# Performance work log

Hardware: AMD Instinct MI355X
Metric: run time of the kernel (lower is better)

Reference implementation:

```python
import jax, jax.numpy as jnp
import numpy as np

T, B, I, H = 512, 64, 1024, 1024


def setup_inputs() -> dict:
    key = jax.random.key(0)
    ks = jax.random.split(key, 7)
    s = 1.0 / np.sqrt(H)
    return {
        "x": jax.random.normal(ks[0], (T, B, I), jnp.float32),
        "h0": jax.random.normal(ks[1], (B, H), jnp.float32),
        "c0": jax.random.normal(ks[2], (B, H), jnp.float32),
        "W_ih": jax.random.normal(ks[3], (4 * H, I), jnp.float32) * s,
        "W_hh": jax.random.normal(ks[4], (4 * H, H), jnp.float32) * s,
        "b_ih": jax.random.normal(ks[5], (4 * H,), jnp.float32) * s,
        "b_hh": jax.random.normal(ks[6], (4 * H,), jnp.float32) * s,
    }


def reference(x, h0, c0, W_ih, W_hh, b_ih, b_hh):
    # Precompute input-to-gate projections for all timesteps at once (same math,
    # just hoisted out of the recurrence): [T, B, 4H]
    gx = jnp.einsum("tbi,gi->tbg", x, W_ih) + b_ih + b_hh

    def step(carry, gx_t):
        h, c = carry
        gates = gx_t + h @ W_hh.T  # [B, 4H]
        i, f, g, o = jnp.split(gates, 4, axis=-1)  # torch LSTMCell gate order
        i = jax.nn.sigmoid(i)
        f = jax.nn.sigmoid(f)
        g = jnp.tanh(g)
        o = jax.nn.sigmoid(o)
        c_new = f * c + i * g
        h_new = o * jnp.tanh(c_new)
        return (h_new, c_new), h_new

    (h_fin, c_fin), outputs = jax.lax.scan(step, (h0, c0), gx)
    return outputs, h_fin, c_fin
```

## Files before the change

### kernel.cpp

```cpp
#include <hip/hip_runtime.h>
#include <hip/hip_bf16.h>


#define BH 65536

typedef __attribute__((ext_vector_type(8))) short bf16x8;
typedef __attribute__((ext_vector_type(4))) float f32x4;

__device__ inline ushort f2bf(float x) {
    __hip_bfloat16 b = __float2bfloat16(x);
    return *(ushort*)&b;
}
__device__ inline float bf2f(ushort u) {
    __hip_bfloat16 b = *(__hip_bfloat16*)&u;
    return __bfloat162float(b);
}

__device__ inline bf16x8 ldh16(const ushort* p) {
    union { unsigned long long q[2]; bf16x8 v; } u;
    u.q[0] = __hip_atomic_load((const unsigned long long*)p,
                               __ATOMIC_RELAXED, __HIP_MEMORY_SCOPE_AGENT);
    u.q[1] = __hip_atomic_load((const unsigned long long*)(p + 4),
                               __ATOMIC_RELAXED, __HIP_MEMORY_SCOPE_AGENT);
    return u.v;
}

__global__ void split_bf16(const float* __restrict__ src,
                           ushort* __restrict__ hi, ushort* __restrict__ lo,
                           long n)
{
    long i0 = ((long)blockIdx.x * blockDim.x + threadIdx.x) * 4;
    long stride = (long)gridDim.x * blockDim.x * 4;
    for (long e = i0; e < n; e += stride) {
        float4 v = *(const float4*)(src + e);
        ushort4 hv, lv;
        hv.x = f2bf(v.x); lv.x = f2bf(v.x - bf2f(hv.x));
        hv.y = f2bf(v.y); lv.y = f2bf(v.y - bf2f(hv.y));
        hv.z = f2bf(v.z); lv.z = f2bf(v.z - bf2f(hv.z));
        hv.w = f2bf(v.w); lv.w = f2bf(v.w - bf2f(hv.w));
        *(ushort4*)(hi + e) = hv;
        *(ushort4*)(lo + e) = lv;
    }
}

__global__ __launch_bounds__(256)
void gx_mfma(const ushort* __restrict__ xhi, const ushort* __restrict__ xlo,
             const ushort* __restrict__ whi, const ushort* __restrict__ wlo,
             const float* __restrict__ bih, const float* __restrict__ bhh,
             float* __restrict__ gxp)
{
    __shared__ short lds[4][4096];
    const int tid  = threadIdx.x;
    const int lane = tid & 63;
    const int w    = tid >> 6;
    const int wm   = w >> 1, wn = w & 1;
    const int mt0  = blockIdx.y * 128;
    const int nt0  = blockIdx.x * 128;

    const int lr_ = w * 16 + (lane >> 2);
    const int lc_ = (lane & 3) * 8;

    f32x4 acc[4][4] = {};

    for (int kt = 0; kt < 1024; kt += 32) {
        uint4 rah[2], ral[2], rbh[2], rbl[2];
        #pragma unroll
        for (int s = 0; s < 2; ++s) {
            size_t ao = (size_t)(mt0 + s * 64 + lr_) * 1024 + kt + lc_;
            size_t bo = (size_t)(nt0 + s * 64 + lr_) * 1024 + kt + lc_;
            rah[s] = *(const uint4*)(xhi + ao);
            ral[s] = *(const uint4*)(xlo + ao);
            rbh[s] = *(const uint4*)(whi + bo);
            rbl[s] = *(const uint4*)(wlo + bo);
        }
        __syncthreads();
        #pragma unroll
        for (int s = 0; s < 2; ++s) {
            int row = s * 64 + lr_;
            int us  = (lane & 3) ^ ((row >> 1) & 3);
            int off = row * 32 + us * 8;
            *(uint4*)&lds[0][off] = rah[s];
            *(uint4*)&lds[1][off] = ral[s];
            *(uint4*)&lds[2][off] = rbh[s];
            *(uint4*)&lds[3][off] = rbl[s];
        }
        __syncthreads();
        bf16x8 ah[4], al[4], bh[4], bl[4];
        #pragma unroll
        for (int f = 0; f < 4; ++f) {
            int arow = wm * 64 + f * 16 + (lane & 15);
            int brow = wn * 64 + f * 16 + (lane & 15);
            int aus  = (lane >> 4) ^ ((arow >> 1) & 3);
            int bus  = (lane >> 4) ^ ((brow >> 1) & 3);
            int ar = arow * 32 + aus * 8;
            int br = brow * 32 + bus * 8;
            ah[f] = *(bf16x8*)&lds[0][ar];
            al[f] = *(bf16x8*)&lds[1][ar];
            bh[f] = *(bf16x8*)&lds[2][br];
            bl[f] = *(bf16x8*)&lds[3][br];
        }
        #pragma unroll
        for (int i = 0; i < 4; ++i)
            #pragma unroll
            for (int j = 0; j < 4; ++j) {
                acc[i][j] = __builtin_amdgcn_mfma_f32_16x16x32_bf16(ah[i], bh[j], acc[i][j], 0, 0, 0);
                acc[i][j] = __builtin_amdgcn_mfma_f32_16x16x32_bf16(ah[i], bl[j], acc[i][j], 0, 0, 0);
                acc[i][j] = __builtin_amdgcn_mfma_f32_16x16x32_bf16(al[i], bh[j], acc[i][j], 0, 0, 0);
            }
    }
    #pragma unroll
    for (int j = 0; j < 4; ++j) {
        int r = nt0 + wn * 64 + j * 16 + (lane & 15);
        float bias = bih[r] + bhh[r];
        int g = r >> 10, u = r & 1023;
        #pragma unroll
        for (int i = 0; i < 4; ++i) {
            #pragma unroll
            for (int e = 0; e < 4; ++e) {
                int m = mt0 + wm * 64 + i * 16 + (lane >> 4) * 4 + e;
                int trel = m >> 6, b = m & 63;
                gxp[(((size_t)trel * 256 + (u >> 2)) * 64 + b) * 16 + g * 4 + (u & 3)]
                    = acc[i][j][e] + bias;
            }
        }
    }
}

#define BM 128
#define BN 128
#define BKg 16

__global__ __launch_bounds__(256, 2)
void gx_gemm(const float* __restrict__ x, const float* __restrict__ Wih,
             const float* __restrict__ bih, const float* __restrict__ bhh,
             float* __restrict__ gxp, int t0)
{
    __shared__ float As[BKg][BM + 4];
    __shared__ float Bs[BKg][BN + 4];
    const int tid  = threadIdx.x;
    const int nblk = blockIdx.x;
    const int mblk = blockIdx.y;
    const int lrow = tid >> 2;
    const int lkq  = (tid & 3) * 4;
    const int ty   = tid >> 4;
    const int tx   = tid & 15;

    const float* xb = x   + ((size_t)t0 * 64 + (size_t)mblk * BM) * 1024;
    const float* wb = Wih + (size_t)nblk * BN * 1024;

    float acc[8][8] = {};
    for (int kt = 0; kt < 1024; kt += BKg) {
        const int k0 = kt + lkq;
        float4 a0 = *(const float4*)(xb + (size_t)lrow        * 1024 + k0);
        float4 a1 = *(const float4*)(xb + (size_t)(lrow + 64) * 1024 + k0);
        float4 b0 = *(const float4*)(wb + (size_t)lrow        * 1024 + k0);
        float4 b1 = *(const float4*)(wb + (size_t)(lrow + 64) * 1024 + k0);
        __syncthreads();
        As[lkq + 0][lrow] = a0.x; As[lkq + 1][lrow] = a0.y;
        As[lkq + 2][lrow] = a0.z; As[lkq + 3][lrow] = a0.w;
        As[lkq + 0][lrow + 64] = a1.x; As[lkq + 1][lrow + 64] = a1.y;
        As[lkq + 2][lrow + 64] = a1.z; As[lkq + 3][lrow + 64] = a1.w;
        Bs[lkq + 0][lrow] = b0.x; Bs[lkq + 1][lrow] = b0.y;
        Bs[lkq + 2][lrow] = b0.z; Bs[lkq + 3][lrow] = b0.w;
        Bs[lkq + 0][lrow + 64] = b1.x; Bs[lkq + 1][lrow + 64] = b1.y;
        Bs[lkq + 2][lrow + 64] = b1.z; Bs[lkq + 3][lrow + 64] = b1.w;
        __syncthreads();
        #pragma unroll
        for (int kk = 0; kk < BKg; ++kk) {
            float4 af0 = *(float4*)&As[kk][ty * 8];
            float4 af1 = *(float4*)&As[kk][ty * 8 + 4];
            float4 bf0 = *(float4*)&Bs[kk][tx * 8];
            float4 bf1 = *(float4*)&Bs[kk][tx * 8 + 4];
            float a[8] = {af0.x, af0.y, af0.z, af0.w, af1.x, af1.y, af1.z, af1.w};
            float b[8] = {bf0.x, bf0.y, bf0.z, bf0.w, bf1.x, bf1.y, bf1.z, bf1.w};
            #pragma unroll
            for (int i = 0; i < 8; ++i)
                #pragma unroll
                for (int j = 0; j < 8; ++j)
                    acc[i][j] += a[i] * b[j];
        }
    }
    float bias[8];
    #pragma unroll
    for (int j = 0; j < 8; ++j) {
        int r = nblk * BN + tx * 8 + j;
        bias[j] = bih[r] + bhh[r];
    }
    #pragma unroll
    for (int i = 0; i < 8; ++i) {
        int ml   = mblk * BM + ty * 8 + i;
        int trel = ml >> 6, b = ml & 63;
        #pragma unroll
        for (int jj = 0; jj < 2; ++jj) {
            int r = nblk * BN + tx * 8 + jj * 4;
            int g = r >> 10, u = r & 1023;
            float4 v = make_float4(acc[i][jj*4+0] + bias[jj*4+0],
                                   acc[i][jj*4+1] + bias[jj*4+1],
                                   acc[i][jj*4+2] + bias[jj*4+2],
                                   acc[i][jj*4+3] + bias[jj*4+3]);
            *(float4*)(gxp + ((((size_t)trel * 256 + (u >> 2)) * 64 + b) << 4) + g * 4) = v;
        }
    }
}

__device__ inline void flagbar(uint token, uint* flags, uint* gen)
{
    __syncthreads();
    const int tid = threadIdx.x;
    if (blockIdx.x == 0) {
        if (tid == 0)
            __hip_atomic_store(&flags[0], token, __ATOMIC_RELAXED, __HIP_MEMORY_SCOPE_AGENT);
        while (__hip_atomic_load(&flags[tid * 16], __ATOMIC_RELAXED, __HIP_MEMORY_SCOPE_AGENT) < token)
            __builtin_amdgcn_s_sleep(2);
        __syncthreads();
        if (tid < 32)
            __hip_atomic_store(&gen[tid * 16], token, __ATOMIC_RELAXED, __HIP_MEMORY_SCOPE_AGENT);
    } else {
        if (tid == 0) {
            __hip_atomic_store(&flags[blockIdx.x * 16], token, __ATOMIC_RELAXED, __HIP_MEMORY_SCOPE_AGENT);
            uint* myg = &gen[(blockIdx.x & 31) * 16];
            while (__hip_atomic_load(myg, __ATOMIC_RELAXED, __HIP_MEMORY_SCOPE_AGENT) < token)
                __builtin_amdgcn_s_sleep(2);
        }
    }
    __syncthreads();
}

__global__ __launch_bounds__(256, 1)
void lstm_persist(const ushort* __restrict__ whh_hi, const ushort* __restrict__ whh_lo,
                  const float* __restrict__ gxp, ushort* __restrict__ hpl,
                  const float* __restrict__ c0, float* __restrict__ cbuf,
                  float* __restrict__ out, int t0, int chunk, uint* bar)
{
    __shared__ float  part[4][64][20];
    __shared__ ushort hstg[64][8];
    const int tid  = threadIdx.x;
    const int lane = tid & 63;
    const int w    = tid >> 6;
    const int cu   = blockIdx.x;
    uint* flags = bar;
    uint* gen   = bar + 4096;

    const int rl    = lane & 15;
    const size_t wrow = (size_t)((rl >> 2) * 1024 + cu * 4 + (rl & 3)) * 1024;
    const int klane = (lane >> 4) * 8;
    const int kbase = w * 256;
    const int bq    = lane & 15;

    bf16x8 a_hi[8], a_lo[8];
    #pragma unroll
    for (int ks = 0; ks < 8; ++ks) {
        int k0 = kbase + ks * 32 + klane;
        a_hi[ks] = *(const bf16x8*)(whh_hi + wrow + k0);
        a_lo[ks] = *(const bf16x8*)(whh_lo + wrow + k0);
    }

    const int eb = tid >> 2, eu = tid & 3;
    const int hcol = cu * 4 + eu;
    float c_reg = (t0 == 0) ? c0[eb * 1024 + hcol] : cbuf[eb * 1024 + hcol];

    for (int t = t0; t < t0 + chunk; ++t) {
        const ushort* hin_hi = hpl + (size_t)(((t + 1) & 1) * 2 + 0) * BH;
        const ushort* hin_lo = hpl + (size_t)(((t + 1) & 1) * 2 + 1) * BH;

        const float* gx = gxp + (((size_t)(t - t0) * 256 + cu) * 64 + eb) * 16;
        float gxv0 = gx[0 + eu], gxv1 = gx[4 + eu];
        float gxv2 = gx[8 + eu], gxv3 = gx[12 + eu];

        f32x4 acc[4] = {};
        #pragma unroll
        for (int ks = 0; ks < 8; ++ks) {
            int k0 = kbase + ks * 32 + klane;
            #pragma unroll
            for (int nt = 0; nt < 4; ++nt) {
                size_t ho = (size_t)(nt * 16 + bq) * 1024 + k0;
                bf16x8 b_hi = ldh16(hin_hi + ho);
                bf16x8 b_lo = ldh16(hin_lo + ho);
                acc[nt] = __builtin_amdgcn_mfma_f32_16x16x32_bf16(a_hi[ks], b_hi, acc[nt], 0, 0, 0);
                acc[nt] = __builtin_amdgcn_mfma_f32_16x16x32_bf16(a_hi[ks], b_lo, acc[nt], 0, 0, 0);
                acc[nt] = __builtin_amdgcn_mfma_f32_16x16x32_bf16(a_lo[ks], b_hi, acc[nt], 0, 0, 0);
            }
        }
        const int r0 = (lane >> 4) * 4;
        #pragma unroll
        for (int nt = 0; nt < 4; ++nt)
            *(f32x4*)&part[w][nt * 16 + bq][r0] = acc[nt];
        __syncthreads();

        float pre0 = part[0][eb][0  + eu] + part[1][eb][0  + eu] + part[2][eb][0  + eu] + part[3][eb][0  + eu] + gxv0;
        float pre1 = part[0][eb][4  + eu] + part[1][eb][4  + eu] + part[2][eb][4  + eu] + part[3][eb][4  + eu] + gxv1;
        float pre2 = part[0][eb][8  + eu] + part[1][eb][8  + eu] + part[2][eb][8  + eu] + part[3][eb][8  + eu] + gxv2;
        float pre3 = part[0][eb][12 + eu] + part[1][eb][12 + eu] + part[2][eb][12 + eu] + part[3][eb][12 + eu] + gxv3;
        float gi = __fdividef(1.0f, 1.0f + __expf(-pre0));
        float gf = __fdividef(1.0f, 1.0f + __expf(-pre1));
        float gg = 1.0f - __fdividef(2.0f, __expf(2.0f * pre2) + 1.0f);
        float go = __fdividef(1.0f, 1.0f + __expf(-pre3));
        c_reg = gf * c_reg + gi * gg;
        float hn = go * (1.0f - __fdividef(2.0f, __expf(2.0f * c_reg) + 1.0f));

        out[((size_t)t * 64 + eb) * 1024 + hcol] = hn;
        ushort hh = f2bf(hn);
        hstg[eb][eu]     = hh;
        hstg[eb][4 + eu] = f2bf(hn - bf2f(hh));
        if (t == 511) {
            out[(size_t)512 * BH + eb * 1024 + hcol]      = hn;
            out[(size_t)512 * BH + BH + eb * 1024 + hcol] = c_reg;
        }
        __syncthreads();
        if (tid < 128) {
            int eb2 = tid >> 1, jj = tid & 1;
            const uint* row = (const uint*)&hstg[eb2][0];
            ushort* hobase = hpl + (size_t)((t & 1) * 2) * BH + eb2 * 1024 + cu * 4;
            __hip_atomic_store((uint*)hobase + jj,      row[jj],
                               __ATOMIC_RELAXED, __HIP_MEMORY_SCOPE_AGENT);
            __hip_atomic_store((uint*)(hobase + BH) + jj, row[2 + jj],
                               __ATOMIC_RELAXED, __HIP_MEMORY_SCOPE_AGENT);
        }
        flagbar((uint)(t + 1), flags, gen);
    }
    if (t0 + chunk < 512)
        cbuf[eb * 1024 + hcol] = c_reg;
}

__global__ __launch_bounds__(256)
void lstm_step_mfma(const ushort* __restrict__ whh_hi, const ushort* __restrict__ whh_lo,
                    const float* __restrict__ gxp,
                    const ushort* __restrict__ hin_hi, const ushort* __restrict__ hin_lo,
                    const float* __restrict__ cprev, float* __restrict__ cbuf,
                    ushort* __restrict__ hout_hi, ushort* __restrict__ hout_lo,
                    float* __restrict__ out, int t, int trel)
{
    __shared__ float part[4][64][20];
    const int tid  = threadIdx.x;
    const int lane = tid & 63;
    const int w    = tid >> 6;
    const int cu   = blockIdx.x;

    const int rl    = lane & 15;
    const size_t wrow = (size_t)((rl >> 2) * 1024 + cu * 4 + (rl & 3)) * 1024;
    const int klane = (lane >> 4) * 8;
    const int kbase = w * 256;
    const int bq    = lane & 15;

    f32x4 acc[4] = {};
    #pragma unroll
    for (int ks = 0; ks < 8; ++ks) {
        int k0 = kbase + ks * 32 + klane;
        bf16x8 a_hi = *(const bf16x8*)(whh_hi + wrow + k0);
        bf16x8 a_lo = *(const bf16x8*)(whh_lo + wrow + k0);
        #pragma unroll
        for (int nt = 0; nt < 4; ++nt) {
            size_t ho = (size_t)(nt * 16 + bq) * 1024 + k0;
            bf16x8 b_hi = *(const bf16x8*)(hin_hi + ho);
            bf16x8 b_lo = *(const bf16x8*)(hin_lo + ho);
            acc[nt] = __builtin_amdgcn_mfma_f32_16x16x32_bf16(a_hi, b_hi, acc[nt], 0, 0, 0);
            acc[nt] = __builtin_amdgcn_mfma_f32_16x16x32_bf16(a_hi, b_lo, acc[nt], 0, 0, 0);
            acc[nt] = __builtin_amdgcn_mfma_f32_16x16x32_bf16(a_lo, b_hi, acc[nt], 0, 0, 0);
        }
    }
    const int r0 = (lane >> 4) * 4;
    #pragma unroll
    for (int nt = 0; nt < 4; ++nt)
        *(f32x4*)&part[w][nt * 16 + bq][r0] = acc[nt];
    __syncthreads();

    const int eb = tid >> 2, eu = tid & 3;
    const float* gx = gxp + (((size_t)trel * 256 + cu) * 64 + eb) * 16;
    float pre[4];
    #pragma unroll
    for (int g = 0; g < 4; ++g) {
        int r = g * 4 + eu;
        pre[g] = part[0][eb][r] + part[1][eb][r] + part[2][eb][r] + part[3][eb][r]
               + gx[g * 4 + eu];
    }
    float gi = __fdividef(1.0f, 1.0f + __expf(-pre[0]));
    float gf = __fdividef(1.0f, 1.0f + __expf(-pre[1]));
    float gg = 1.0f - __fdividef(2.0f, __expf(2.0f * pre[2]) + 1.0f);
    float go = __fdividef(1.0f, 1.0f + __expf(-pre[3]));
    float c_reg = cprev[eb * 1024 + cu * 4 + eu];
    c_reg = gf * c_reg + gi * gg;
    float hn = go * (1.0f - __fdividef(2.0f, __expf(2.0f * c_reg) + 1.0f));

    int hcol = cu * 4 + eu;
    cbuf[eb * 1024 + hcol] = c_reg;
    out[((size_t)t * 64 + eb) * 1024 + hcol] = hn;
    ushort hh = f2bf(hn);
    hout_hi[eb * 1024 + hcol] = hh;
    hout_lo[eb * 1024 + hcol] = f2bf(hn - bf2f(hh));
    if (t == 511) {
        out[(size_t)512 * BH + eb * 1024 + hcol]      = hn;
        out[(size_t)512 * BH + BH + eb * 1024 + hcol] = c_reg;
    }
}

extern "C" void kernel_launch(void* const* d_in, const int* in_sizes, int n_in,
                              void* d_out, int out_size, void* d_ws, size_t ws_size,
                              hipStream_t stream)
{
    const float* x   = (const float*)d_in[0];
    const float* h0  = (const float*)d_in[1];
    const float* c0  = (const float*)d_in[2];
    const float* Wih = (const float*)d_in[3];
    const float* Whh = (const float*)d_in[4];
    const float* bih = (const float*)d_in[5];
    const float* bhh = (const float*)d_in[6];
    float* out = (float*)d_out;

    char* ws = (char*)d_ws;
    float* cbuf = (float*)ws;

    const size_t FIXED0 = 262144 + 4 * 8388608L + 524288;
    const size_t FIXED  = FIXED0 + 32768;
    const long   PER    = 2 * 131072L + 1048576L;
    long Tc = ((long)ws_size - (long)FIXED) / PER;

    if (Tc >= 2) {
        if (Tc > 512) Tc = 512;
        Tc &= ~1L;
        ushort* wih_hi = (ushort*)(ws + 262144);
        ushort* wih_lo = wih_hi + 4194304;
        ushort* whh_hi = wih_lo + 4194304;
        ushort* whh_lo = whh_hi + 4194304;
        ushort* hpl    = whh_lo + 4194304;
        uint*   bar    = (uint*)(ws + FIXED0);
        char*   var    = ws + FIXED;
        ushort* xhi    = (ushort*)var;
        ushort* xlo    = (ushort*)(var + Tc * 131072);
        float*  gxp    = (float*)(var + Tc * 262144);

        hipMemsetAsync(bar, 0, 32768, stream);
        split_bf16<<<dim3(2048), dim3(256), 0, stream>>>(Wih, wih_hi, wih_lo, 4194304L);
        split_bf16<<<dim3(2048), dim3(256), 0, stream>>>(Whh, whh_hi, whh_lo, 4194304L);
        split_bf16<<<dim3(64),   dim3(256), 0, stream>>>(h0, hpl + 2 * BH, hpl + 3 * BH, (long)BH);

        bool coop_ok = true;
        for (int t0 = 0; t0 < 512; t0 += (int)Tc) {
            int chunk = (512 - t0 < (int)Tc) ? (512 - t0) : (int)Tc;
            split_bf16<<<dim3(4096), dim3(256), 0, stream>>>(
                x + (size_t)t0 * BH, xhi, xlo, (long)chunk * BH);
            gx_mfma<<<dim3(32, chunk / 2), dim3(256), 0, stream>>>(
                xhi, xlo, wih_hi, wih_lo, bih, bhh, gxp);
            if (coop_ok) {
                void* args[] = {(void*)&whh_hi, (void*)&whh_lo, (void*)&gxp,
                                (void*)&hpl, (void*)&c0, (void*)&cbuf,
                                (void*)&out, (void*)&t0, (void*)&chunk,
                                (void*)&bar};
                hipError_t e = hipLaunchCooperativeKernel(
                    (void*)lstm_persist, dim3(256), dim3(256), args, 0, stream);
                if (e != hipSuccess) { (void)hipGetLastError(); coop_ok = false; }
            }
            if (!coop_ok) {
                for (int trel = 0; trel < chunk; ++trel) {
                    int t = t0 + trel;
                    int rb = (t + 1) & 1, wb = t & 1;
                    const float* cp = (t == 0) ? c0 : cbuf;
                    lstm_step_mfma<<<dim3(256), dim3(256), 0, stream>>>(
                        whh_hi, whh_lo, gxp,
                        hpl + rb * 2 * BH, hpl + rb * 2 * BH + BH,
                        cp, cbuf,
                        hpl + wb * 2 * BH, hpl + wb * 2 * BH + BH,
                        out, t, trel);
                }
            }
        }
    } else {
        ushort* whh_hi = (ushort*)(ws + 262144);
        ushort* whh_lo = whh_hi + 4194304;
        ushort* hpl    = whh_lo + 4194304;
        const size_t FIXED2 = 262144 + 2 * 8388608L + 524288;
        float* gxp = (float*)(ws + FIXED2);
        long Tc2 = ((long)ws_size - (long)FIXED2) / 1048576L;
        if (Tc2 > 512) Tc2 = 512;
        Tc2 &= ~1L;
        if (Tc2 < 2) Tc2 = 2;

        split_bf16<<<dim3(2048), dim3(256), 0, stream>>>(Whh, whh_hi, whh_lo, 4194304L);
        split_bf16<<<dim3(64),   dim3(256), 0, stream>>>(h0, hpl + 2 * BH, hpl + 3 * BH, (long)BH);

        for (int t0 = 0; t0 < 512; t0 += (int)Tc2) {
            int chunk = (512 - t0 < (int)Tc2) ? (512 - t0) : (int)Tc2;
            gx_gemm<<<dim3(32, chunk * 64 / BM), dim3(256), 0, stream>>>(
                x, Wih, bih, bhh, gxp, t0);
            for (int trel = 0; trel < chunk; ++trel) {
                int t = t0 + trel;
                int rb = (t + 1) & 1, wb = t & 1;
                const float* cp = (t == 0) ? c0 : cbuf;
                lstm_step_mfma<<<dim3(256), dim3(256), 0, stream>>>(
                    whh_hi, whh_lo, gxp,
                    hpl + rb * 2 * BH, hpl + rb * 2 * BH + BH,
                    cp, cbuf,
                    hpl + wb * 2 * BH, hpl + wb * 2 * BH + BH,
                    out, t, trel);
            }
        }
    }
}
```

Before: 11.59 ms.

## Restructure persistent LSTM kernel to 64 large blocks with LDS-staged hidden state

The persistent recurrence kernel now runs 64 blocks of 1024 threads instead of 256 blocks of 256. Each block owns 16 hidden units across all four gates. Each step, the block cooperatively loads the full bf16 hi/lo hidden state into swizzled shared memory in four quarter-K chunks, prefetching the next chunk while MFMAs run. Weights are streamed from global memory every step rather than held in registers. The grid barrier now involves 64 blocks, which cuts barrier and synchronisation cost and redundant hidden-state reads, at the price of re-reading W_hh each step and more __syncthreads per step.

```diff
diff --git a/kernel.cpp b/kernel.cpp
--- a/kernel.cpp
+++ b/kernel.cpp
@@ -6,6 +6,7 @@
 
 typedef __attribute__((ext_vector_type(8))) short bf16x8;
 typedef __attribute__((ext_vector_type(4))) float f32x4;
+typedef unsigned long long ull;
 
 __device__ inline ushort f2bf(float x) {
     __hip_bfloat16 b = __float2bfloat16(x);
@@ -14,15 +15,6 @@
 __device__ inline float bf2f(ushort u) {
     __hip_bfloat16 b = *(__hip_bfloat16*)&u;
     return __bfloat162float(b);
-}
-
-__device__ inline bf16x8 ldh16(const ushort* p) {
-    union { unsigned long long q[2]; bf16x8 v; } u;
-    u.q[0] = __hip_atomic_load((const unsigned long long*)p,
-                               __ATOMIC_RELAXED, __HIP_MEMORY_SCOPE_AGENT);
-    u.q[1] = __hip_atomic_load((const unsigned long long*)(p + 4),
-                               __ATOMIC_RELAXED, __HIP_MEMORY_SCOPE_AGENT);
-    return u.v;
 }
 
 __global__ void split_bf16(const float* __restrict__ src,
@@ -203,15 +195,17 @@
     }
 }
 
-__device__ inline void flagbar(uint token, uint* flags, uint* gen)
+__device__ inline void flagbar64(uint token, uint* flags, uint* gen)
 {
     __syncthreads();
     const int tid = threadIdx.x;
     if (blockIdx.x == 0) {
         if (tid == 0)
             __hip_atomic_store(&flags[0], token, __ATOMIC_RELAXED, __HIP_MEMORY_SCOPE_AGENT);
-        while (__hip_atomic_load(&flags[tid * 16], __ATOMIC_RELAXED, __HIP_MEMORY_SCOPE_AGENT) < token)
-            __builtin_amdgcn_s_sleep(2);
+        if (tid < 64) {
+            while (__hip_atomic_load(&flags[tid * 16], __ATOMIC_RELAXED, __HIP_MEMORY_SCOPE_AGENT) < token)
+                __builtin_amdgcn_s_sleep(2);
+        }
         __syncthreads();
         if (tid < 32)
             __hip_atomic_store(&gen[tid * 16], token, __ATOMIC_RELAXED, __HIP_MEMORY_SCOPE_AGENT);
@@ -226,100 +220,138 @@
     __syncthreads();
 }
 
-__global__ __launch_bounds__(256, 1)
+__global__ __launch_bounds__(1024, 4)
 void lstm_persist(const ushort* __restrict__ whh_hi, const ushort* __restrict__ whh_lo,
                   const float* __restrict__ gxp, ushort* __restrict__ hpl,
                   const float* __restrict__ c0, float* __restrict__ cbuf,
                   float* __restrict__ out, int t0, int chunk, uint* bar)
 {
-    __shared__ float  part[4][64][20];
-    __shared__ ushort hstg[64][8];
+    __shared__ uint4  hstage[2][2048];
+    __shared__ float  pre[64][65];
+    __shared__ ushort hstg2[64][32];
+
     const int tid  = threadIdx.x;
     const int lane = tid & 63;
-    const int w    = tid >> 6;
+    const int wid  = tid >> 6;
+    const int g    = wid >> 2;
+    const int wc   = wid & 3;
     const int cu   = blockIdx.x;
     uint* flags = bar;
     uint* gen   = bar + 4096;
 
-    const int rl    = lane & 15;
-    const size_t wrow = (size_t)((rl >> 2) * 1024 + cu * 4 + (rl & 3)) * 1024;
-    const int klane = (lane >> 4) * 8;
-    const int kbase = w * 256;
-    const int bq    = lane & 15;
-
-    bf16x8 a_hi[8], a_lo[8];
-    #pragma unroll
-    for (int ks = 0; ks < 8; ++ks) {
-        int k0 = kbase + ks * 32 + klane;
-        a_hi[ks] = *(const bf16x8*)(whh_hi + wrow + k0);
-        a_lo[ks] = *(const bf16x8*)(whh_lo + wrow + k0);
-    }
-
-    const int eb = tid >> 2, eu = tid & 3;
-    const int hcol = cu * 4 + eu;
-    float c_reg = (t0 == 0) ? c0[eb * 1024 + hcol] : cbuf[eb * 1024 + hcol];
+    const int ul_a  = lane & 15;
+    const int kl    = (lane >> 4) * 8;
+    const int batch = wc * 16 + (lane & 15);
+    const ushort* wbase_hi = whh_hi + (size_t)(g * 1024 + cu * 16 + ul_a) * 1024;
+    const ushort* wbase_lo = whh_lo + (size_t)(g * 1024 + cu * 16 + ul_a) * 1024;
+
+    const int ul = tid & 15, b = tid >> 4;
+    const int hcol = cu * 16 + ul;
+    float c_reg = (t0 == 0) ? c0[b * 1024 + hcol] : cbuf[b * 1024 + hcol];
+
+    const int sb = tid >> 4;
+    const int su = (tid & 15) * 2;
 
     for (int t = t0; t < t0 + chunk; ++t) {
         const ushort* hin_hi = hpl + (size_t)(((t + 1) & 1) * 2 + 0) * BH;
         const ushort* hin_lo = hpl + (size_t)(((t + 1) & 1) * 2 + 1) * BH;
 
-        const float* gx = gxp + (((size_t)(t - t0) * 256 + cu) * 64 + eb) * 16;
-        float gxv0 = gx[0 + eu], gxv1 = gx[4 + eu];
-        float gxv2 = gx[8 + eu], gxv3 = gx[12 + eu];
-
-        f32x4 acc[4] = {};
-        #pragma unroll
-        for (int ks = 0; ks < 8; ++ks) {
-            int k0 = kbase + ks * 32 + klane;
+        const float* gx = gxp + (((size_t)(t - t0) * 256 + cu * 4 + (ul >> 2)) * 64 + b) * 16;
+        int ul2 = ul & 3;
+        float gxv0 = gx[0 + ul2], gxv1 = gx[4 + ul2];
+        float gxv2 = gx[8 + ul2], gxv3 = gx[12 + ul2];
+
+        f32x4 acc = {};
+        ull rh[4], rl[4];
+        {
+            const ull* shi = (const ull*)(hin_hi + sb * 1024 + su * 8);
+            const ull* slo = (const ull*)(hin_lo + sb * 1024 + su * 8);
             #pragma unroll
-            for (int nt = 0; nt < 4; ++nt) {
-                size_t ho = (size_t)(nt * 16 + bq) * 1024 + k0;
-                bf16x8 b_hi = ldh16(hin_hi + ho);
-                bf16x8 b_lo = ldh16(hin_lo + ho);
-                acc[nt] = __builtin_amdgcn_mfma_f32_16x16x32_bf16(a_hi[ks], b_hi, acc[nt], 0, 0, 0);
-                acc[nt] = __builtin_amdgcn_mfma_f32_16x16x32_bf16(a_hi[ks], b_lo, acc[nt], 0, 0, 0);
-                acc[nt] = __builtin_amdgcn_mfma_f32_16x16x32_bf16(a_lo[ks], b_hi, acc[nt], 0, 0, 0);
-            }
-        }
-        const int r0 = (lane >> 4) * 4;
-        #pragma unroll
-        for (int nt = 0; nt < 4; ++nt)
-            *(f32x4*)&part[w][nt * 16 + bq][r0] = acc[nt];
-        __syncthreads();
-
-        float pre0 = part[0][eb][0  + eu] + part[1][eb][0  + eu] + part[2][eb][0  + eu] + part[3][eb][0  + eu] + gxv0;
-        float pre1 = part[0][eb][4  + eu] + part[1][eb][4  + eu] + part[2][eb][4  + eu] + part[3][eb][4  + eu] + gxv1;
-        float pre2 = part[0][eb][8  + eu] + part[1][eb][8  + eu] + part[2][eb][8  + eu] + part[3][eb][8  + eu] + gxv2;
-        float pre3 = part[0][eb][12 + eu] + part[1][eb][12 + eu] + part[2][eb][12 + eu] + part[3][eb][12 + eu] + gxv3;
-        float gi = __fdividef(1.0f, 1.0f + __expf(-pre0));
-        float gf = __fdividef(1.0f, 1.0f + __expf(-pre1));
-        float gg = 1.0f - __fdividef(2.0f, __expf(2.0f * pre2) + 1.0f);
-        float go = __fdividef(1.0f, 1.0f + __expf(-pre3));
+            for (int i = 0; i < 4; ++i) {
+                rh[i] = __hip_atomic_load(shi + i, __ATOMIC_RELAXED, __HIP_MEMORY_SCOPE_AGENT);
+                rl[i] = __hip_atomic_load(slo + i, __ATOMIC_RELAXED, __HIP_MEMORY_SCOPE_AGENT);
+            }
+        }
+        for (int q = 0; q < 4; ++q) {
+            __syncthreads();
+            {
+                ull* hs0 = (ull*)&hstage[0][0];
+                ull* hs1 = (ull*)&hstage[1][0];
+                int u0 = (su)     ^ (sb & 7);
+                int u1 = (su + 1) ^ (sb & 7);
+                hs0[sb * 64 + u0 * 2 + 0] = rh[0];
+                hs0[sb * 64 + u0 * 2 + 1] = rh[1];
+                hs0[sb * 64 + u1 * 2 + 0] = rh[2];
+                hs0[sb * 64 + u1 * 2 + 1] = rh[3];
+                hs1[sb * 64 + u0 * 2 + 0] = rl[0];
+                hs1[sb * 64 + u0 * 2 + 1] = rl[1];
+                hs1[sb * 64 + u1 * 2 + 0] = rl[2];
+                hs1[sb * 64 + u1 * 2 + 1] = rl[3];
+            }
+            __syncthreads();
+            if (q < 3) {
+                const ull* shi = (const ull*)(hin_hi + sb * 1024 + (q + 1) * 256 + su * 8);
+                const ull* slo = (const ull*)(hin_lo + sb * 1024 + (q + 1) * 256 + su * 8);
+                #pragma unroll
+                for (int i = 0; i < 4; ++i) {
+                    rh[i] = __hip_atomic_load(shi + i, __ATOMIC_RELAXED, __HIP_MEMORY_SCOPE_AGENT);
+                    rl[i] = __hip_atomic_load(slo + i, __ATOMIC_RELAXED, __HIP_MEMORY_SCOPE_AGENT);
+                }
+            }
+            #pragma unroll
+            for (int ks = 0; ks < 8; ++ks) {
+                const ushort* wp = wbase_hi + q * 256 + ks * 32 + kl;
+                bf16x8 a_hi = *(const bf16x8*)wp;
+                bf16x8 a_lo = *(const bf16x8*)(wbase_lo + q * 256 + ks * 32 + kl);
+                int u16  = ks * 4 + (lane >> 4);
+                int phys = u16 ^ (batch & 7);
+                bf16x8 b_hi = *(bf16x8*)&hstage[0][batch * 32 + phys];
+                bf16x8 b_lo = *(bf16x8*)&hstage[1][batch * 32 + phys];
+                acc = __builtin_amdgcn_mfma_f32_16x16x32_bf16(a_hi, b_hi, acc, 0, 0, 0);
+                acc = __builtin_amdgcn_mfma_f32_16x16x32_bf16(a_hi, b_lo, acc, 0, 0, 0);
+                acc = __builtin_amdgcn_mfma_f32_16x16x32_bf16(a_lo, b_hi, acc, 0, 0, 0);
+            }
+        }
+        #pragma unroll
+        for (int e = 0; e < 4; ++e)
+            pre[g * 16 + (lane >> 4) * 4 + e][wc * 16 + (lane & 15)] = acc[e];
+        __syncthreads();
+
+        float p0 = pre[ 0 + ul][b] + gxv0;
+        float p1 = pre[16 + ul][b] + gxv1;
+        float p2 = pre[32 + ul][b] + gxv2;
+        float p3 = pre[48 + ul][b] + gxv3;
+        float gi = __fdividef(1.0f, 1.0f + __expf(-p0));
+        float gf = __fdividef(1.0f, 1.0f + __expf(-p1));
+        float gg = 1.0f - __fdividef(2.0f, __expf(2.0f * p2) + 1.0f);
+        float go = __fdividef(1.0f, 1.0f + __expf(-p3));
         c_reg = gf * c_reg + gi * gg;
         float hn = go * (1.0f - __fdividef(2.0f, __expf(2.0f * c_reg) + 1.0f));
 
-        out[((size_t)t * 64 + eb) * 1024 + hcol] = hn;
+        out[((size_t)t * 64 + b) * 1024 + hcol] = hn;
         ushort hh = f2bf(hn);
-        hstg[eb][eu]     = hh;
-        hstg[eb][4 + eu] = f2bf(hn - bf2f(hh));
+        hstg2[b][ul]      = hh;
+        hstg2[b][16 + ul] = f2bf(hn - bf2f(hh));
         if (t == 511) {
-            out[(size_t)512 * BH + eb * 1024 + hcol]      = hn;
-            out[(size_t)512 * BH + BH + eb * 1024 + hcol] = c_reg;
-        }
-        __syncthreads();
-        if (tid < 128) {
-            int eb2 = tid >> 1, jj = tid & 1;
-            const uint* row = (const uint*)&hstg[eb2][0];
-            ushort* hobase = hpl + (size_t)((t & 1) * 2) * BH + eb2 * 1024 + cu * 4;
-            __hip_atomic_store((uint*)hobase + jj,      row[jj],
-                               __ATOMIC_RELAXED, __HIP_MEMORY_SCOPE_AGENT);
-            __hip_atomic_store((uint*)(hobase + BH) + jj, row[2 + jj],
-                               __ATOMIC_RELAXED, __HIP_MEMORY_SCOPE_AGENT);
-        }
-        flagbar((uint)(t + 1), flags, gen);
+            out[(size_t)512 * BH + b * 1024 + hcol]      = hn;
+            out[(size_t)512 * BH + BH + b * 1024 + hcol] = c_reg;
+        }
+        __syncthreads();
+        {
+            int pb = tid >> 4, j = tid & 15;
+            const uint* row = (const uint*)&hstg2[pb][0];
+            ushort* ho = hpl + (size_t)((t & 1) * 2) * BH + pb * 1024 + cu * 16;
+            if (j < 8)
+                __hip_atomic_store((uint*)ho + j, row[j],
+                                   __ATOMIC_RELAXED, __HIP_MEMORY_SCOPE_AGENT);
+            else
+                __hip_atomic_store((uint*)(ho + BH) + (j - 8), row[j],
+                                   __ATOMIC_RELAXED, __HIP_MEMORY_SCOPE_AGENT);
+        }
+        flagbar64((uint)(t + 1), flags, gen);
     }
     if (t0 + chunk < 512)
-        cbuf[eb * 1024 + hcol] = c_reg;
+        cbuf[b * 1024 + hcol] = c_reg;
 }
 
 __global__ __launch_bounds__(256)
@@ -446,7 +478,7 @@
                                 (void*)&out, (void*)&t0, (void*)&chunk,
                                 (void*)&bar};
                 hipError_t e = hipLaunchCooperativeKernel(
-                    (void*)lstm_persist, dim3(256), dim3(256), args, 0, stream);
+                    (void*)lstm_persist, dim3(64), dim3(1024), args, 0, stream);
                 if (e != hipSuccess) { (void)hipGetLastError(); coop_ok = false; }
             }
             if (!coop_ok) {
```

After: 20.61 ms. +77.9%, slower.

## Split persistent LSTM step across 16 waves per block, one N-tile each

Applied to the files above, without the earlier changes.

The persistent recurrent kernel now launches 1024 threads per block instead of 256, giving each of 16 waves one K-quarter and one batch tile rather than four tiles per wave. The aim is to shorten the serial per-step MFMA and load chain and hide the latency of the atomic h loads with more waves in flight. Only the first 256 threads run the gate nonlinearity and state update, so the remaining threads sit idle at the barriers. The wider block raises register pressure per CU and may reduce the redundant A-fragment reuse, since each wave still holds its full W_hh slice in registers.

```diff
diff --git a/kernel.cpp b/kernel.cpp
--- a/kernel.cpp
+++ b/kernel.cpp
@@ -6,6 +6,7 @@
 
 typedef __attribute__((ext_vector_type(8))) short bf16x8;
 typedef __attribute__((ext_vector_type(4))) float f32x4;
+typedef unsigned long long ull;
 
 __device__ inline ushort f2bf(float x) {
     __hip_bfloat16 b = __float2bfloat16(x);
@@ -17,10 +18,10 @@
 }
 
 __device__ inline bf16x8 ldh16(const ushort* p) {
-    union { unsigned long long q[2]; bf16x8 v; } u;
-    u.q[0] = __hip_atomic_load((const unsigned long long*)p,
+    union { ull q[2]; bf16x8 v; } u;
+    u.q[0] = __hip_atomic_load((const ull*)p,
                                __ATOMIC_RELAXED, __HIP_MEMORY_SCOPE_AGENT);
-    u.q[1] = __hip_atomic_load((const unsigned long long*)(p + 4),
+    u.q[1] = __hip_atomic_load((const ull*)(p + 4),
                                __ATOMIC_RELAXED, __HIP_MEMORY_SCOPE_AGENT);
     return u.v;
 }
@@ -210,8 +211,10 @@
     if (blockIdx.x == 0) {
         if (tid == 0)
             __hip_atomic_store(&flags[0], token, __ATOMIC_RELAXED, __HIP_MEMORY_SCOPE_AGENT);
-        while (__hip_atomic_load(&flags[tid * 16], __ATOMIC_RELAXED, __HIP_MEMORY_SCOPE_AGENT) < token)
-            __builtin_amdgcn_s_sleep(2);
+        if (tid < 256) {
+            while (__hip_atomic_load(&flags[tid * 16], __ATOMIC_RELAXED, __HIP_MEMORY_SCOPE_AGENT) < token)
+                __builtin_amdgcn_s_sleep(2);
+        }
         __syncthreads();
         if (tid < 32)
             __hip_atomic_store(&gen[tid * 16], token, __ATOMIC_RELAXED, __HIP_MEMORY_SCOPE_AGENT);
@@ -226,7 +229,7 @@
     __syncthreads();
 }
 
-__global__ __launch_bounds__(256, 1)
+__global__ __launch_bounds__(1024, 4)
 void lstm_persist(const ushort* __restrict__ whh_hi, const ushort* __restrict__ whh_lo,
                   const float* __restrict__ gxp, ushort* __restrict__ hpl,
                   const float* __restrict__ c0, float* __restrict__ cbuf,
@@ -236,7 +239,9 @@
     __shared__ ushort hstg[64][8];
     const int tid  = threadIdx.x;
     const int lane = tid & 63;
-    const int w    = tid >> 6;
+    const int wid  = tid >> 6;
+    const int kq   = wid >> 2;
+    const int nt   = wid & 3;
     const int cu   = blockIdx.x;
     uint* flags = bar;
     uint* gen   = bar + 4096;
@@ -244,7 +249,7 @@
     const int rl    = lane & 15;
     const size_t wrow = (size_t)((rl >> 2) * 1024 + cu * 4 + (rl & 3)) * 1024;
     const int klane = (lane >> 4) * 8;
-    const int kbase = w * 256;
+    const int kbase = kq * 256;
     const int bq    = lane & 15;
 
     bf16x8 a_hi[8], a_lo[8];
@@ -255,56 +260,58 @@
         a_lo[ks] = *(const bf16x8*)(whh_lo + wrow + k0);
     }
 
-    const int eb = tid >> 2, eu = tid & 3;
+    const int eb = (tid >> 2) & 63, eu = tid & 3;
     const int hcol = cu * 4 + eu;
-    float c_reg = (t0 == 0) ? c0[eb * 1024 + hcol] : cbuf[eb * 1024 + hcol];
+    float c_reg = 0.0f;
+    if (tid < 256)
+        c_reg = (t0 == 0) ? c0[eb * 1024 + hcol] : cbuf[eb * 1024 + hcol];
 
     for (int t = t0; t < t0 + chunk; ++t) {
         const ushort* hin_hi = hpl + (size_t)(((t + 1) & 1) * 2 + 0) * BH;
         const ushort* hin_lo = hpl + (size_t)(((t + 1) & 1) * 2 + 1) * BH;
 
-        const float* gx = gxp + (((size_t)(t - t0) * 256 + cu) * 64 + eb) * 16;
-        float gxv0 = gx[0 + eu], gxv1 = gx[4 + eu];
-        float gxv2 = gx[8 + eu], gxv3 = gx[12 + eu];
-
-        f32x4 acc[4] = {};
+        float gxv0 = 0, gxv1 = 0, gxv2 = 0, gxv3 = 0;
+        if (tid < 256) {
+            const float* gx = gxp + (((size_t)(t - t0) * 256 + cu) * 64 + eb) * 16;
+            gxv0 = gx[0 + eu]; gxv1 = gx[4 + eu];
+            gxv2 = gx[8 + eu]; gxv3 = gx[12 + eu];
+        }
+
+        f32x4 acc = {};
         #pragma unroll
         for (int ks = 0; ks < 8; ++ks) {
             int k0 = kbase + ks * 32 + klane;
-            #pragma unroll
-            for (int nt = 0; nt < 4; ++nt) {
-                size_t ho = (size_t)(nt * 16 + bq) * 1024 + k0;
-                bf16x8 b_hi = ldh16(hin_hi + ho);
-                bf16x8 b_lo = ldh16(hin_lo + ho);
-                acc[nt] = __builtin_amdgcn_mfma_f32_16x16x32_bf16(a_hi[ks], b_hi, acc[nt], 0, 0, 0);
-                acc[nt] = __builtin_amdgcn_mfma_f32_16x16x32_bf16(a_hi[ks], b_lo, acc[nt], 0, 0, 0);
-                acc[nt] = __builtin_amdgcn_mfma_f32_16x16x32_bf16(a_lo[ks], b_hi, acc[nt], 0, 0, 0);
+            size_t ho = (size_t)(nt * 16 + bq) * 1024 + k0;
+            bf16x8 b_hi = ldh16(hin_hi + ho);
+            bf16x8 b_lo = ldh16(hin_lo + ho);
+            acc = __builtin_amdgcn_mfma_f32_16x16x32_bf16(a_hi[ks], b_hi, acc, 0, 0, 0);
+            acc = __builtin_amdgcn_mfma_f32_16x16x32_bf16(a_hi[ks], b_lo, acc, 0, 0, 0);
+            acc = __builtin_amdgcn_mfma_f32_16x16x32_bf16(a_lo[ks], b_hi, acc, 0, 0, 0);
+        }
+        const int r0 = (lane >> 4) * 4;
+        *(f32x4*)&part[kq][nt * 16 + bq][r0] = acc;
+        __syncthreads();
+
+        if (tid < 256) {
+            float pre0 = part[0][eb][0  + eu] + part[1][eb][0  + eu] + part[2][eb][0  + eu] + part[3][eb][0  + eu] + gxv0;
+            float pre1 = part[0][eb][4  + eu] + part[1][eb][4  + eu] + part[2][eb][4  + eu] + part[3][eb][4  + eu] + gxv1;
+            float pre2 = part[0][eb][8  + eu] + part[1][eb][8  + eu] + part[2][eb][8  + eu] + part[3][eb][8  + eu] + gxv2;
+            float pre3 = part[0][eb][12 + eu] + part[1][eb][12 + eu] + part[2][eb][12 + eu] + part[3][eb][12 + eu] + gxv3;
+            float gi = __fdividef(1.0f, 1.0f + __expf(-pre0));
+            float gf = __fdividef(1.0f, 1.0f + __expf(-pre1));
+            float gg = 1.0f - __fdividef(2.0f, __expf(2.0f * pre2) + 1.0f);
+            float go = __fdividef(1.0f, 1.0f + __expf(-pre3));
+            c_reg = gf * c_reg + gi * gg;
+            float hn = go * (1.0f - __fdividef(2.0f, __expf(2.0f * c_reg) + 1.0f));
+
+            out[((size_t)t * 64 + eb) * 1024 + hcol] = hn;
+            ushort hh = f2bf(hn);
+            hstg[eb][eu]     = hh;
+            hstg[eb][4 + eu] = f2bf(hn - bf2f(hh));
+            if (t == 511) {
+                out[(size_t)512 * BH + eb * 1024 + hcol]      = hn;
+                out[(size_t)512 * BH + BH + eb * 1024 + hcol] = c_reg;
             }
-        }
-        const int r0 = (lane >> 4) * 4;
-        #pragma unroll
-        for (int nt = 0; nt < 4; ++nt)
-            *(f32x4*)&part[w][nt * 16 + bq][r0] = acc[nt];
-        __syncthreads();
-
-        float pre0 = part[0][eb][0  + eu] + part[1][eb][0  + eu] + part[2][eb][0  + eu] + part[3][eb][0  + eu] + gxv0;
-        float pre1 = part[0][eb][4  + eu] + part[1][eb][4  + eu] + part[2][eb][4  + eu] + part[3][eb][4  + eu] + gxv1;
-        float pre2 = part[0][eb][8  + eu] + part[1][eb][8  + eu] + part[2][eb][8  + eu] + part[3][eb][8  + eu] + gxv2;
-        float pre3 = part[0][eb][12 + eu] + part[1][eb][12 + eu] + part[2][eb][12 + eu] + part[3][eb][12 + eu] + gxv3;
-        float gi = __fdividef(1.0f, 1.0f + __expf(-pre0));
-        float gf = __fdividef(1.0f, 1.0f + __expf(-pre1));
-        float gg = 1.0f - __fdividef(2.0f, __expf(2.0f * pre2) + 1.0f);
-        float go = __fdividef(1.0f, 1.0f + __expf(-pre3));
-        c_reg = gf * c_reg + gi * gg;
-        float hn = go * (1.0f - __fdividef(2.0f, __expf(2.0f * c_reg) + 1.0f));
-
-        out[((size_t)t * 64 + eb) * 1024 + hcol] = hn;
-        ushort hh = f2bf(hn);
-        hstg[eb][eu]     = hh;
-        hstg[eb][4 + eu] = f2bf(hn - bf2f(hh));
-        if (t == 511) {
-            out[(size_t)512 * BH + eb * 1024 + hcol]      = hn;
-            out[(size_t)512 * BH + BH + eb * 1024 + hcol] = c_reg;
         }
         __syncthreads();
         if (tid < 128) {
@@ -318,7 +325,7 @@
         }
         flagbar((uint)(t + 1), flags, gen);
     }
-    if (t0 + chunk < 512)
+    if (t0 + chunk < 512 && tid < 256)
         cbuf[eb * 1024 + hcol] = c_reg;
 }
 
@@ -446,7 +453,7 @@
                                 (void*)&out, (void*)&t0, (void*)&chunk,
                                 (void*)&bar};
                 hipError_t e = hipLaunchCooperativeKernel(
-                    (void*)lstm_persist, dim3(256), dim3(256), args, 0, stream);
+                    (void*)lstm_persist, dim3(256), dim3(1024), args, 0, stream);
                 if (e != hipSuccess) { (void)hipGetLastError(); coop_ok = false; }
             }
             if (!coop_ok) {
```

Result: faster. 11.32 ms (-2.3%).
